# Kernel optimization log

Hardware: AMD Instinct MI355X
Metric: run time of the kernel (lower is better)

The kernel has to match this reference:

```python
import jax, jax.numpy as jnp
import numpy as np

# dims
B, CIN, H, W = 64, 96, 28, 28
E = 4            # num_experts
EXPAND = 6
HID = CIN * EXPAND   # 576
K = 5
STRIDE = 1
PAD = K // 2
RED = max(1, int(CIN * 0.25))      # SE reduced dim = 24
RHID = max(16, CIN // 4)           # routing hidden = 24
COUT = 96
EPS = 1e-3


def setup_inputs() -> dict:
    key = jax.random.key(0)
    ks = jax.random.split(key, 12)
    rn = lambda k, shape, s=0.05: jax.random.normal(k, shape, jnp.float32) * s
    return dict(
        x=jax.random.normal(ks[0], (B, CIN, H, W), jnp.float32),
        # routing net: Linear(CIN->RHID) + ReLU + Linear(RHID->E)
        r_w1=rn(ks[1], (RHID, CIN)), r_b1=jnp.zeros((RHID,), jnp.float32),
        r_w2=rn(ks[2], (E, RHID)), r_b2=jnp.zeros((E,), jnp.float32),
        # expand 1x1 conv (no bias)
        exp_w=rn(ks[3], (HID, CIN)),
        bn1_g=jnp.ones((HID,), jnp.float32), bn1_b=jnp.zeros((HID,), jnp.float32),
        bn1_m=jnp.zeros((HID,), jnp.float32), bn1_v=jnp.ones((HID,), jnp.float32),
        # MoE depthwise expert kernels [E, HID, K, K]
        dw_w=rn(ks[4], (E, HID, K, K)),
        bn2_g=jnp.ones((HID,), jnp.float32), bn2_b=jnp.zeros((HID,), jnp.float32),
        bn2_m=jnp.zeros((HID,), jnp.float32), bn2_v=jnp.ones((HID,), jnp.float32),
        # squeeze-excitation 1x1 convs (with bias)
        se_w1=rn(ks[5], (RED, HID)), se_b1=jnp.zeros((RED,), jnp.float32),
        se_w2=rn(ks[6], (HID, RED)), se_b2=jnp.zeros((HID,), jnp.float32),
        # MoE pointwise expert kernels [E, COUT, HID]
        pw_w=rn(ks[7], (E, COUT, HID)),
        bn3_g=jnp.ones((COUT,), jnp.float32), bn3_b=jnp.zeros((COUT,), jnp.float32),
        bn3_m=jnp.zeros((COUT,), jnp.float32), bn3_v=jnp.ones((COUT,), jnp.float32),
    )


def _bn(y, g, b, m, v):
    sh = (1, -1, 1, 1)
    inv = g.reshape(sh) * jax.lax.rsqrt(v.reshape(sh) + EPS)
    return (y - m.reshape(sh)) * inv + b.reshape(sh)


def _dwconv_per_sample(x, kernels):
    # x [b,c,h,w], kernels [b,c,k,k] -> per-sample depthwise conv
    c = x.shape[1]
    def one(xi, wi):
        return jax.lax.conv_general_dilated(
            xi[None], wi[:, None],  # [1,c,h,w], [c,1,k,k]
            window_strides=(STRIDE, STRIDE),
            padding=[(PAD, PAD), (PAD, PAD)],
            feature_group_count=c,
            dimension_numbers=('NCHW', 'OIHW', 'NCHW'))[0]
    return jax.vmap(one)(x, kernels)


def reference(x, r_w1, r_b1, r_w2, r_b2, exp_w,
              bn1_g, bn1_b, bn1_m, bn1_v, dw_w,
              bn2_g, bn2_b, bn2_m, bn2_v,
              se_w1, se_b1, se_w2, se_b2, pw_w,
              bn3_g, bn3_b, bn3_m, bn3_v):
    silu = jax.nn.silu
    # routing: global avg pool -> MLP -> softmax (temperature = 1.0)
    pool = x.mean(axis=(2, 3))                          # [b, cin]
    hdn = jax.nn.relu(pool @ r_w1.T + r_b1)             # [b, rhid]
    logits = (hdn @ r_w2.T + r_b2).astype(jnp.float32)  # [b, E]
    rw = jax.nn.softmax(logits, axis=-1).astype(x.dtype)
    # expand 1x1 conv + BN + SiLU
    out = jnp.einsum('oc,bchw->bohw', exp_w, x)         # [b, hid, h, w]
    out = silu(_bn(out, bn1_g, bn1_b, bn1_m, bn1_v))
    # MoE depthwise: aggregate per-sample kernels, per-sample depthwise conv
    kern = jnp.einsum('be,eckl->bckl', rw, dw_w)        # [b, hid, k, k]
    out = _dwconv_per_sample(out, kern)
    out = silu(_bn(out, bn2_g, bn2_b, bn2_m, bn2_v))
    # squeeze-excitation
    s = out.mean(axis=(2, 3))                           # [b, hid]
    z = silu(s @ se_w1.T + se_b1)                       # [b, red]
    sc = jax.nn.sigmoid(z @ se_w2.T + se_b2)            # [b, hid]
    out = out * sc[:, :, None, None]
    # MoE pointwise projection: per-sample 1x1 conv weights
    wpw = jnp.einsum('be,eoc->boc', rw, pw_w)           # [b, cout, hid]
    out = jnp.einsum('boc,bchw->bohw', wpw, out)        # [b, cout, h, w]
    out = _bn(out, bn3_g, bn3_b, bn3_m, bn3_v)
    # residual (stride==1, cin==cout); stochastic depth is identity in eval
    return x + out
```

## Files before the change

kernel.cpp:

```cpp
#include <hip/hip_runtime.h>
#include <hip/hip_bf16.h>
#include <math.h>

#define B 64
#define CIN 96
#define HH 28
#define WW 28
#define NPIX 784
#define E 4
#define HID 576
#define RED 24
#define RHID 24
#define COUT 96
#define EPS 1e-3f

typedef __attribute__((ext_vector_type(8))) short short8v;
typedef __attribute__((ext_vector_type(4))) float f32x4;

__device__ __forceinline__ float sigmoidf_(float v) { return 1.0f / (1.0f + __expf(-v)); }

__device__ __forceinline__ unsigned short f2bf(float v) {
    __hip_bfloat16 h = __float2bfloat16(v);
    return *reinterpret_cast<unsigned short*>(&h);
}

__global__ __launch_bounds__(256) void k_pool(const float* __restrict__ x, float* __restrict__ pool) {
    int row = blockIdx.x * 4 + (threadIdx.x >> 6);
    int lane = threadIdx.x & 63;
    const float4* xr = reinterpret_cast<const float4*>(x + (size_t)row * NPIX);
    float s = 0.f;
    for (int i = lane; i < 196; i += 64) {
        float4 v = xr[i];
        s += v.x + v.y + v.z + v.w;
    }
#pragma unroll
    for (int off = 32; off > 0; off >>= 1) s += __shfl_down(s, off);
    if (lane == 0) pool[row] = s * (1.0f / NPIX);
}

__global__ __launch_bounds__(256) void k_mlp(const float* __restrict__ pool,
                                             const float* __restrict__ r_w1, const float* __restrict__ r_b1,
                                             const float* __restrict__ r_w2, const float* __restrict__ r_b2,
                                             float* __restrict__ rw) {
    __shared__ float w1[RHID * CIN];
    __shared__ float b1s[RHID];
    __shared__ float w2[E * RHID];
    __shared__ float b2s[E];
    __shared__ float pl[B * CIN];
    int tid = threadIdx.x;
    for (int i = tid; i < RHID * CIN; i += 256) w1[i] = r_w1[i];
    if (tid < RHID) b1s[tid] = r_b1[tid];
    if (tid < E * RHID) w2[tid] = r_w2[tid];
    if (tid < E) b2s[tid] = r_b2[tid];
    for (int i = tid; i < B * CIN; i += 256) pl[i] = pool[i];
    __syncthreads();
    if (tid < B) {
        const float* p = pl + tid * CIN;
        float hdn[RHID];
#pragma unroll
        for (int r = 0; r < RHID; ++r) {
            float a = b1s[r];
            for (int c = 0; c < CIN; ++c) a += p[c] * w1[r * CIN + c];
            hdn[r] = fmaxf(a, 0.f);
        }
        float lg[E];
        float mx = -1e30f;
#pragma unroll
        for (int e = 0; e < E; ++e) {
            float a = b2s[e];
#pragma unroll
            for (int r = 0; r < RHID; ++r) a += hdn[r] * w2[e * RHID + r];
            lg[e] = a;
            mx = fmaxf(mx, a);
        }
        float den = 0.f;
#pragma unroll
        for (int e = 0; e < E; ++e) { lg[e] = __expf(lg[e] - mx); den += lg[e]; }
#pragma unroll
        for (int e = 0; e < E; ++e) rw[tid * E + e] = lg[e] / den;
    }
}

__global__ void k_wcvt(const float* __restrict__ w, unsigned short* __restrict__ wb) {
    int i = blockIdx.x * blockDim.x + threadIdx.x;
    if (i < HID * CIN) wb[i] = f2bf(w[i]);
}

__global__ __launch_bounds__(256) void k_expand_mfma(
    const float* __restrict__ x, const unsigned short* __restrict__ w_bf,
    const float* __restrict__ bn1_g, const float* __restrict__ bn1_b,
    const float* __restrict__ bn1_m, const float* __restrict__ bn1_v,
    __hip_bfloat16* __restrict__ hid) {
    int nc = blockIdx.x;
    int b = blockIdx.y;
    int tid = threadIdx.x;
    int lane = tid & 63, wv = tid >> 6;
    int col = lane & 15, g = lane >> 4;
    __shared__ unsigned short xt[96 * 116];
    __shared__ float inv1s[HID], sh1s[HID];

    for (int i = tid; i < HID; i += 256) {
        float inv = bn1_g[i] * rsqrtf(bn1_v[i] + EPS);
        inv1s[i] = inv;
        sh1s[i] = bn1_b[i] - bn1_m[i] * inv;
    }
    const float* xb = x + (size_t)b * CIN * NPIX + nc * 112;
    for (int i = tid; i < 96 * 112; i += 256) {
        int c = i / 112, p = i % 112;
        xt[c * 116 + p] = f2bf(xb[c * NPIX + p]);
    }
    __syncthreads();

    const short8v* wv8 = reinterpret_cast<const short8v*>(w_bf);
    for (int nf = 0; nf < 7; ++nf) {
        int pcol = nf * 16 + col;
        short8v bfr[3];
#pragma unroll
        for (int kk = 0; kk < 3; ++kk) {
            int k0 = kk * 32 + 8 * g;
#pragma unroll
            for (int j = 0; j < 8; ++j) bfr[kk][j] = (short)xt[(k0 + j) * 116 + pcol];
        }
        int px = nc * 112 + pcol;
#pragma unroll
        for (int mi = 0; mi < 9; ++mi) {
            int mb = (wv * 9 + mi) * 16;
            f32x4 acc = {0.f, 0.f, 0.f, 0.f};
#pragma unroll
            for (int kk = 0; kk < 3; ++kk) {
                short8v af = wv8[((mb + col) * 96 + kk * 32 + 8 * g) >> 3];
                acc = __builtin_amdgcn_mfma_f32_16x16x32_bf16(af, bfr[kk], acc, 0, 0, 0);
            }
#pragma unroll
            for (int r = 0; r < 4; ++r) {
                int oc = mb + 4 * g + r;
                float t = acc[r] * inv1s[oc] + sh1s[oc];
                float u = t * sigmoidf_(t);
                hid[((size_t)b * HID + oc) * NPIX + px] = __float2bfloat16(u);
            }
        }
    }
}

__global__ __launch_bounds__(256, 2) void k_dw(
    __hip_bfloat16* __restrict__ hid, const float* __restrict__ rw,
    const float* __restrict__ dw_w,
    const float* __restrict__ bn2_g, const float* __restrict__ bn2_b,
    const float* __restrict__ bn2_m, const float* __restrict__ bn2_v,
    float* __restrict__ s_out) {
    const int CT = 16;
    int ct = blockIdx.x;
    int b = blockIdx.y;
    int tid = threadIdx.x;
    int cb = ct * CT;
    __shared__ float plane[CT][NPIX];
    __shared__ float kl[CT][25];
    __shared__ float ssum[CT];
    __hip_bfloat16* hb = hid + ((size_t)b * HID + cb) * NPIX;
    for (int i = tid; i < CT * NPIX; i += 256) plane[i / NPIX][i % NPIX] = __bfloat162float(hb[i]);
    {
        float rwl[E];
#pragma unroll
        for (int e = 0; e < E; ++e) rwl[e] = rw[b * E + e];
        for (int i = tid; i < CT * 25; i += 256) {
            int ci = i / 25, j = i % 25;
            int c = cb + ci;
            float a = 0.f;
#pragma unroll
            for (int e = 0; e < E; ++e) a += rwl[e] * dw_w[((size_t)e * HID + c) * 25 + j];
            float inv2 = bn2_g[c] * rsqrtf(bn2_v[c] + EPS);
            kl[ci][j] = a * inv2;
        }
    }
    if (tid < CT) ssum[tid] = 0.f;
    __syncthreads();
    for (int pass = 0; pass < 2; ++pass) {
        int col = pass * 256 + tid;
        if (col < CT * WW) {
            int ci = col / WW, w = col % WW;
            float k[25];
#pragma unroll
            for (int j = 0; j < 25; ++j) k[j] = kl[ci][j];
            float win[5][5];
#pragma unroll
            for (int i = 0; i < 5; ++i) {
                int hr = i - 2;
#pragma unroll
                for (int j = 0; j < 5; ++j) {
                    int wc = w - 2 + j;
                    win[i][j] = (hr >= 0 && hr < HH && wc >= 0 && wc < WW) ? plane[ci][hr * WW + wc] : 0.f;
                }
            }
            int c = cb + ci;
            float inv2 = bn2_g[c] * rsqrtf(bn2_v[c] + EPS);
            float sh2 = bn2_b[c] - bn2_m[c] * inv2;
            float csum = 0.f;
#pragma unroll
            for (int h = 0; h < HH; ++h) {
                float o = 0.f;
#pragma unroll
                for (int i = 0; i < 5; ++i)
#pragma unroll
                    for (int j = 0; j < 5; ++j) o += win[i][j] * k[i * 5 + j];
                float t = o + sh2;
                float u = t * sigmoidf_(t);
                csum += u;
                hb[ci * NPIX + h * WW + w] = __float2bfloat16(u);
#pragma unroll
                for (int i = 0; i < 4; ++i)
#pragma unroll
                    for (int j = 0; j < 5; ++j) win[i][j] = win[i + 1][j];
                int hn = h + 3;
#pragma unroll
                for (int j = 0; j < 5; ++j) {
                    int wc = w - 2 + j;
                    win[4][j] = (hn < HH && wc >= 0 && wc < WW) ? plane[ci][hn * WW + wc] : 0.f;
                }
            }
            atomicAdd(&ssum[ci], csum);
        }
    }
    __syncthreads();
    if (tid < CT) s_out[(size_t)b * HID + cb + tid] = ssum[tid] * (1.0f / NPIX);
}

__global__ __launch_bounds__(256) void k_se_wpw(
    const float* __restrict__ s, const float* __restrict__ se_w1,
    const float* __restrict__ se_b1, const float* __restrict__ se_w2,
    const float* __restrict__ se_b2, const float* __restrict__ rw,
    const float* __restrict__ pw_w,
    const float* __restrict__ bn3_g, const float* __restrict__ bn3_v,
    unsigned short* __restrict__ wpw) {
    int seg = blockIdx.x;
    int b = blockIdx.y;
    int tid = threadIdx.x;
    __shared__ float sl[HID];
    __shared__ float zl[RED];
    __shared__ float scl[HID];
    for (int i = tid; i < HID; i += 256) sl[i] = s[(size_t)b * HID + i];
    __syncthreads();
    if (tid < RED) {
        float a = se_b1[tid];
        for (int c = 0; c < HID; ++c) a += sl[c] * se_w1[tid * HID + c];
        zl[tid] = a * sigmoidf_(a);
    }
    __syncthreads();
    for (int c = tid; c < HID; c += 256) {
        float a = se_b2[c];
#pragma unroll
        for (int r = 0; r < RED; ++r) a += zl[r] * se_w2[c * RED + r];
        scl[c] = sigmoidf_(a);
    }
    __syncthreads();
    float rwl[E];
#pragma unroll
    for (int e = 0; e < E; ++e) rwl[e] = rw[b * E + e];
    unsigned short* wb = wpw + (size_t)b * COUT * HID;
    for (int i = tid; i < 16 * HID; i += 256) {
        int o = seg * 16 + i / HID, c = i % HID;
        float a = 0.f;
#pragma unroll
        for (int e = 0; e < E; ++e) a += rwl[e] * pw_w[((size_t)e * COUT + o) * HID + c];
        float inv3 = bn3_g[o] * rsqrtf(bn3_v[o] + EPS);
        wb[o * HID + c] = f2bf(a * inv3 * scl[c]);
    }
}

__global__ __launch_bounds__(448) void k_pw_mfma(
    const __hip_bfloat16* __restrict__ hid, const unsigned short* __restrict__ wpw,
    const float* __restrict__ x,
    const float* __restrict__ bn3_g, const float* __restrict__ bn3_b,
    const float* __restrict__ bn3_m, const float* __restrict__ bn3_v,
    float* __restrict__ out) {
    int nc = blockIdx.x;
    int b = blockIdx.y;
    int tid = threadIdx.x;
    int lane = tid & 63, nf = tid >> 6;
    int col = lane & 15, g = lane >> 4;
    __shared__ unsigned short Wl[96 * 104];
    __shared__ unsigned short Ht[96 * 116];
    __shared__ float inv3s[COUT], sh3s[COUT];
    if (tid < COUT) {
        float inv = bn3_g[tid] * rsqrtf(bn3_v[tid] + EPS);
        inv3s[tid] = inv;
        sh3s[tid] = bn3_b[tid] - bn3_m[tid] * inv;
    }
    const unsigned short* hb = (const unsigned short*)hid + (size_t)b * HID * NPIX + nc * 112;
    const unsigned short* wb = wpw + (size_t)b * COUT * HID;
    f32x4 acc[6];
#pragma unroll
    for (int m = 0; m < 6; ++m) acc[m] = (f32x4){0.f, 0.f, 0.f, 0.f};

    for (int ks = 0; ks < 6; ++ks) {
        __syncthreads();
        for (int i = tid; i < 96 * 48; i += 448) {
            int m = i / 48, k2 = i % 48;
            *(uint*)&Wl[m * 104 + 2 * k2] = *(const uint*)&wb[m * HID + ks * 96 + 2 * k2];
        }
        for (int i = tid; i < 96 * 56; i += 448) {
            int k = i / 56, p2 = i % 56;
            *(uint*)&Ht[k * 116 + 2 * p2] = *(const uint*)&hb[((size_t)(ks * 96 + k)) * NPIX + 2 * p2];
        }
        __syncthreads();
#pragma unroll
        for (int kk = 0; kk < 3; ++kk) {
            int k0 = kk * 32 + 8 * g;
            short8v bfr;
#pragma unroll
            for (int j = 0; j < 8; ++j) bfr[j] = (short)Ht[(k0 + j) * 116 + nf * 16 + col];
#pragma unroll
            for (int m = 0; m < 6; ++m) {
                short8v af = *(const short8v*)&Wl[(m * 16 + col) * 104 + kk * 32 + 8 * g];
                acc[m] = __builtin_amdgcn_mfma_f32_16x16x32_bf16(af, bfr, acc[m], 0, 0, 0);
            }
        }
    }
    int px = nc * 112 + nf * 16 + col;
#pragma unroll
    for (int m = 0; m < 6; ++m) {
#pragma unroll
        for (int r = 0; r < 4; ++r) {
            int oc = m * 16 + 4 * g + r;
            size_t off = ((size_t)b * COUT + oc) * NPIX + px;
            out[off] = acc[m][r] + sh3s[oc] + x[off];
        }
    }
}

extern "C" void kernel_launch(void* const* d_in, const int* in_sizes, int n_in,
                              void* d_out, int out_size, void* d_ws, size_t ws_size,
                              hipStream_t stream) {
    const float* x     = (const float*)d_in[0];
    const float* r_w1  = (const float*)d_in[1];
    const float* r_b1  = (const float*)d_in[2];
    const float* r_w2  = (const float*)d_in[3];
    const float* r_b2  = (const float*)d_in[4];
    const float* exp_w = (const float*)d_in[5];
    const float* bn1_g = (const float*)d_in[6];
    const float* bn1_b = (const float*)d_in[7];
    const float* bn1_m = (const float*)d_in[8];
    const float* bn1_v = (const float*)d_in[9];
    const float* dw_w  = (const float*)d_in[10];
    const float* bn2_g = (const float*)d_in[11];
    const float* bn2_b = (const float*)d_in[12];
    const float* bn2_m = (const float*)d_in[13];
    const float* bn2_v = (const float*)d_in[14];
    const float* se_w1 = (const float*)d_in[15];
    const float* se_b1 = (const float*)d_in[16];
    const float* se_w2 = (const float*)d_in[17];
    const float* se_b2 = (const float*)d_in[18];
    const float* pw_w  = (const float*)d_in[19];
    const float* bn3_g = (const float*)d_in[20];
    const float* bn3_b = (const float*)d_in[21];
    const float* bn3_m = (const float*)d_in[22];
    const float* bn3_v = (const float*)d_in[23];
    float* out = (float*)d_out;

    char* ws = (char*)d_ws;
    float* rw                 = (float*)(ws + 0);
    float* pool               = (float*)(ws + 1024);
    float* s                  = (float*)(ws + 26624);
    unsigned short* exp_w_bf  = (unsigned short*)(ws + 174336);
    unsigned short* wpw_bf    = (unsigned short*)(ws + 285184);
    __hip_bfloat16* hid       = (__hip_bfloat16*)(ws + 7363328);

    k_pool<<<B * CIN / 4, 256, 0, stream>>>(x, pool);
    k_mlp<<<1, 256, 0, stream>>>(pool, r_w1, r_b1, r_w2, r_b2, rw);
    k_wcvt<<<(HID * CIN + 255) / 256, 256, 0, stream>>>(exp_w, exp_w_bf);
    k_expand_mfma<<<dim3(7, B), 256, 0, stream>>>(x, exp_w_bf, bn1_g, bn1_b, bn1_m, bn1_v, hid);
    k_dw<<<dim3(36, B), 256, 0, stream>>>(hid, rw, dw_w, bn2_g, bn2_b, bn2_m, bn2_v, s);
    k_se_wpw<<<dim3(6, B), 256, 0, stream>>>(s, se_w1, se_b1, se_w2, se_b2, rw, pw_w, bn3_g, bn3_v, wpw_bf);
    k_pw_mfma<<<dim3(7, B), 448, 0, stream>>>(hid, wpw_bf, x, bn3_g, bn3_b, bn3_m, bn3_v, out);
}
```

Baseline: 335.2 us.

## Store depthwise planes as zero-padded bf16 in LDS and use one thread per column

After: 361.5 us. 7.9% more time.

```diff
diff --git a/kernel.cpp b/kernel.cpp
--- a/kernel.cpp
+++ b/kernel.cpp
@@ -24,6 +24,11 @@
     return *reinterpret_cast<unsigned short*>(&h);
 }
 
+__device__ __forceinline__ float bf2f(unsigned short u) {
+    unsigned int w = ((unsigned int)u) << 16;
+    return *reinterpret_cast<float*>(&w);
+}
+
 __global__ __launch_bounds__(256) void k_pool(const float* __restrict__ x, float* __restrict__ pool) {
     int row = blockIdx.x * 4 + (threadIdx.x >> 6);
     int lane = threadIdx.x & 63;
@@ -105,9 +110,12 @@
         sh1s[i] = bn1_b[i] - bn1_m[i] * inv;
     }
     const float* xb = x + (size_t)b * CIN * NPIX + nc * 112;
-    for (int i = tid; i < 96 * 112; i += 256) {
-        int c = i / 112, p = i % 112;
-        xt[c * 116 + p] = f2bf(xb[c * NPIX + p]);
+    for (int i = tid; i < 96 * 28; i += 256) {
+        int c = i / 28, q = i % 28;
+        float4 v = *reinterpret_cast<const float4*>(&xb[c * NPIX + q * 4]);
+        ushort4 s;
+        s.x = f2bf(v.x); s.y = f2bf(v.y); s.z = f2bf(v.z); s.w = f2bf(v.w);
+        *reinterpret_cast<ushort4*>(&xt[c * 116 + q * 4]) = s;
     }
     __syncthreads();
 
@@ -142,84 +150,86 @@
     }
 }
 
-__global__ __launch_bounds__(256, 2) void k_dw(
+#define CT 16
+#define PRS 34
+#define PCS (32 * PRS + 22)
+__global__ __launch_bounds__(448) void k_dw(
     __hip_bfloat16* __restrict__ hid, const float* __restrict__ rw,
     const float* __restrict__ dw_w,
     const float* __restrict__ bn2_g, const float* __restrict__ bn2_b,
     const float* __restrict__ bn2_m, const float* __restrict__ bn2_v,
     float* __restrict__ s_out) {
-    const int CT = 16;
     int ct = blockIdx.x;
     int b = blockIdx.y;
     int tid = threadIdx.x;
     int cb = ct * CT;
-    __shared__ float plane[CT][NPIX];
+    __shared__ unsigned short P[CT * PCS];
     __shared__ float kl[CT][25];
     __shared__ float ssum[CT];
     __hip_bfloat16* hb = hid + ((size_t)b * HID + cb) * NPIX;
-    for (int i = tid; i < CT * NPIX; i += 256) plane[i / NPIX][i % NPIX] = __bfloat162float(hb[i]);
+
+    for (int i = tid; i < CT * PCS / 2; i += 448) reinterpret_cast<unsigned int*>(P)[i] = 0u;
+    if (tid < CT) ssum[tid] = 0.f;
+    __syncthreads();
+    const unsigned int* hb32 = reinterpret_cast<const unsigned int*>(hb);
+    for (int i = tid; i < CT * (NPIX / 2); i += 448) {
+        int ci = i / (NPIX / 2), p2 = i % (NPIX / 2);
+        int px = 2 * p2;
+        int h = px / WW, w = px % WW;
+        *reinterpret_cast<unsigned int*>(&P[ci * PCS + (h + 2) * PRS + (w + 2)]) = hb32[i];
+    }
     {
         float rwl[E];
 #pragma unroll
         for (int e = 0; e < E; ++e) rwl[e] = rw[b * E + e];
-        for (int i = tid; i < CT * 25; i += 256) {
+        for (int i = tid; i < CT * 25; i += 448) {
             int ci = i / 25, j = i % 25;
             int c = cb + ci;
             float a = 0.f;
 #pragma unroll
             for (int e = 0; e < E; ++e) a += rwl[e] * dw_w[((size_t)e * HID + c) * 25 + j];
-            float inv2 = bn2_g[c] * rsqrtf(bn2_v[c] + EPS);
-            kl[ci][j] = a * inv2;
-        }
-    }
-    if (tid < CT) ssum[tid] = 0.f;
-    __syncthreads();
-    for (int pass = 0; pass < 2; ++pass) {
-        int col = pass * 256 + tid;
-        if (col < CT * WW) {
-            int ci = col / WW, w = col % WW;
-            float k[25];
-#pragma unroll
-            for (int j = 0; j < 25; ++j) k[j] = kl[ci][j];
-            float win[5][5];
-#pragma unroll
-            for (int i = 0; i < 5; ++i) {
-                int hr = i - 2;
-#pragma unroll
-                for (int j = 0; j < 5; ++j) {
-                    int wc = w - 2 + j;
-                    win[i][j] = (hr >= 0 && hr < HH && wc >= 0 && wc < WW) ? plane[ci][hr * WW + wc] : 0.f;
-                }
-            }
-            int c = cb + ci;
-            float inv2 = bn2_g[c] * rsqrtf(bn2_v[c] + EPS);
-            float sh2 = bn2_b[c] - bn2_m[c] * inv2;
-            float csum = 0.f;
-#pragma unroll
-            for (int h = 0; h < HH; ++h) {
-                float o = 0.f;
-#pragma unroll
-                for (int i = 0; i < 5; ++i)
-#pragma unroll
-                    for (int j = 0; j < 5; ++j) o += win[i][j] * k[i * 5 + j];
-                float t = o + sh2;
-                float u = t * sigmoidf_(t);
-                csum += u;
-                hb[ci * NPIX + h * WW + w] = __float2bfloat16(u);
-#pragma unroll
-                for (int i = 0; i < 4; ++i)
-#pragma unroll
-                    for (int j = 0; j < 5; ++j) win[i][j] = win[i + 1][j];
-                int hn = h + 3;
-#pragma unroll
-                for (int j = 0; j < 5; ++j) {
-                    int wc = w - 2 + j;
-                    win[4][j] = (hn < HH && wc >= 0 && wc < WW) ? plane[ci][hn * WW + wc] : 0.f;
-                }
-            }
-            atomicAdd(&ssum[ci], csum);
-        }
-    }
+            kl[ci][j] = a * (bn2_g[c] * rsqrtf(bn2_v[c] + EPS));
+        }
+    }
+    __syncthreads();
+
+    int ci = tid / WW, w = tid % WW;
+    const unsigned short* Pc = P + ci * PCS;
+    float k[25];
+#pragma unroll
+    for (int j = 0; j < 25; ++j) k[j] = kl[ci][j];
+    int c = cb + ci;
+    float inv2 = bn2_g[c] * rsqrtf(bn2_v[c] + EPS);
+    float sh2 = bn2_b[c] - bn2_m[c] * inv2;
+
+    float win[5][5];
+#pragma unroll
+    for (int i = 0; i < 5; ++i)
+#pragma unroll
+        for (int j = 0; j < 5; ++j) win[i][j] = bf2f(Pc[i * PRS + w + j]);
+
+    float csum = 0.f;
+#pragma unroll
+    for (int h = 0; h < HH; ++h) {
+        float o = 0.f;
+#pragma unroll
+        for (int i = 0; i < 5; ++i)
+#pragma unroll
+            for (int j = 0; j < 5; ++j) o += win[i][j] * k[i * 5 + j];
+        float t = o + sh2;
+        float u = t * sigmoidf_(t);
+        csum += u;
+        hb[ci * NPIX + h * WW + w] = __float2bfloat16(u);
+        if (h < HH - 1) {
+#pragma unroll
+            for (int i = 0; i < 4; ++i)
+#pragma unroll
+                for (int j = 0; j < 5; ++j) win[i][j] = win[i + 1][j];
+#pragma unroll
+            for (int j = 0; j < 5; ++j) win[4][j] = bf2f(Pc[(h + 5) * PRS + w + j]);
+        }
+    }
+    atomicAdd(&ssum[ci], csum);
     __syncthreads();
     if (tid < CT) s_out[(size_t)b * HID + cb + tid] = ssum[tid] * (1.0f / NPIX);
 }
@@ -368,7 +378,7 @@
     k_mlp<<<1, 256, 0, stream>>>(pool, r_w1, r_b1, r_w2, r_b2, rw);
     k_wcvt<<<(HID * CIN + 255) / 256, 256, 0, stream>>>(exp_w, exp_w_bf);
     k_expand_mfma<<<dim3(7, B), 256, 0, stream>>>(x, exp_w_bf, bn1_g, bn1_b, bn1_m, bn1_v, hid);
-    k_dw<<<dim3(36, B), 256, 0, stream>>>(hid, rw, dw_w, bn2_g, bn2_b, bn2_m, bn2_v, s);
+    k_dw<<<dim3(36, B), 448, 0, stream>>>(hid, rw, dw_w, bn2_g, bn2_b, bn2_m, bn2_v, s);
     k_se_wpw<<<dim3(6, B), 256, 0, stream>>>(s, se_w1, se_b1, se_w2, se_b2, rw, pw_w, bn3_g, bn3_v, wpw_bf);
     k_pw_mfma<<<dim3(7, B), 448, 0, stream>>>(hid, wpw_bf, x, bn3_g, bn3_b, bn3_m, bn3_v, out);
 }
```
